# Kernel tuning notes

Hardware: AMD Instinct MI355X
Metric: run time of the kernel (lower is better)

The kernel has to match this reference:

```python
import jax, jax.numpy as jnp
import numpy as np

N = 8192
D = 128
LMBD = 0.1
SPARSITY = 0.99  # fraction of zero entries in A


def setup_inputs() -> dict:
    key = jax.random.key(0)
    kA, kW = jax.random.split(key)
    u = jax.random.uniform(kA, (N, N), dtype=jnp.float32)
    A = jnp.where(u > SPARSITY, u, 0.0)
    W = jax.random.normal(kW, (N, D), dtype=jnp.float32) * 0.02
    b = jnp.zeros((D,), dtype=jnp.float32)
    return {"A": A, "W": W, "b": b}


def reference(A, W, b):
    # model(tf.eye(N)) with Dense(d) == eye(N) @ W + b == W + b  -> [N, d]
    Y = W + b
    # main loss: 0.5 * sum(mask * (A - Y Y^T)^2), mask = (A > 0)
    R = A - jnp.matmul(Y, Y.T)  # [N, N]
    main_loss = 0.5 * jnp.sum(jnp.where(A > 0, R * R, 0.0))
    # reg loss: lmbd/2 * ||Y||_F^2
    reg_loss = 0.5 * LMBD * jnp.sum(Y * Y)
    return main_loss + reg_loss
```

## Files before the change

kernel.cpp:

```cpp
#include <hip/hip_runtime.h>

#define N 8192
#define D 128
#define MAXNZ 256

__device__ __forceinline__ float wave_reduce(float p) {
    #pragma unroll
    for (int off = 32; off > 0; off >>= 1)
        p += __shfl_xor(p, off, 64);
    return p;
}

__global__ __launch_bounds__(256, 8)
void gf_main_kernel(const float* __restrict__ A,
                    const float* __restrict__ W,
                    const float* __restrict__ b,
                    float* __restrict__ partials) {
    __shared__ int   s_col[4][MAXNZ];
    __shared__ float s_val[4][MAXNZ];
    __shared__ float s_bsum[4];

    const int lane = threadIdx.x & 63;
    const int w    = threadIdx.x >> 6;
    const int row  = blockIdx.x * 4 + w;

    const float2 bb = ((const float2*)b)[lane];
    float2 yi = ((const float2*)(W + (size_t)row * D))[lane];
    yi.x += bb.x; yi.y += bb.y;

    const float4* Arow = (const float4*)(A + (size_t)row * N);
    const unsigned long long ltmask = (lane == 63) ? ~0ull >> 1 : (1ull << lane) - 1ull;
    int cnt = 0;
    for (int it = 0; it < N / 256; ++it) {
        const float4 a4 = Arow[it * 64 + lane];
        const float av[4] = {a4.x, a4.y, a4.z, a4.w};
        #pragma unroll
        for (int q = 0; q < 4; ++q) {
            const unsigned long long m = __ballot(av[q] > 0.0f);
            if (av[q] > 0.0f) {
                const int pos = cnt + __popcll(m & ((1ull << lane) - 1ull));
                if (pos < MAXNZ) {
                    s_col[w][pos] = it * 256 + lane * 4 + q;
                    s_val[w][pos] = av[q];
                }
            }
            cnt += __popcll(m);
        }
    }
    if (cnt > MAXNZ) cnt = MAXNZ;
    __syncthreads();

    float acc = 0.0f;
    for (int t = 0; t < cnt; t += 4) {
        float p[4];
        float av[4];
        #pragma unroll
        for (int k = 0; k < 4; ++k) {
            const bool valid = (t + k) < cnt;
            const int  idx   = valid ? (t + k) : 0;
            const int  j     = s_col[w][idx];
            av[k]            = valid ? s_val[w][idx] : 0.0f;
            const float2 yj  = ((const float2*)(W + (size_t)j * D))[lane];
            p[k] = yi.x * (yj.x + bb.x) + yi.y * (yj.y + bb.y);
        }
        #pragma unroll
        for (int off = 32; off > 0; off >>= 1) {
            #pragma unroll
            for (int k = 0; k < 4; ++k)
                p[k] += __shfl_xor(p[k], off, 64);
        }
        #pragma unroll
        for (int k = 0; k < 4; ++k) {
            if ((t + k) < cnt) {
                const float r = av[k] - p[k];
                acc += r * r;
            }
        }
    }

    const float reg = wave_reduce(yi.x * yi.x + yi.y * yi.y);
    const float total = 0.5f * acc + 0.05f * reg;
    if (lane == 0) s_bsum[w] = total;
    __syncthreads();
    if (threadIdx.x == 0)
        partials[blockIdx.x] = s_bsum[0] + s_bsum[1] + s_bsum[2] + s_bsum[3];
}

__global__ __launch_bounds__(256)
void gf_reduce_kernel(const float* __restrict__ partials, float* __restrict__ out) {
    __shared__ float s_ws[4];
    const int lane = threadIdx.x & 63;
    const int w    = threadIdx.x >> 6;
    float s = 0.0f;
    for (int i = threadIdx.x; i < N / 4; i += 256) s += partials[i];
    s = wave_reduce(s);
    if (lane == 0) s_ws[w] = s;
    __syncthreads();
    if (threadIdx.x == 0) out[0] = s_ws[0] + s_ws[1] + s_ws[2] + s_ws[3];
}

extern "C" void kernel_launch(void* const* d_in, const int* in_sizes, int n_in,
                              void* d_out, int out_size, void* d_ws, size_t ws_size,
                              hipStream_t stream) {
    const float* A = (const float*)d_in[0];
    const float* W = (const float*)d_in[1];
    const float* b = (const float*)d_in[2];
    float* out = (float*)d_out;
    float* partials = (float*)d_ws;

    gf_main_kernel<<<dim3(N / 4), dim3(256), 0, stream>>>(A, W, b, partials);
    gf_reduce_kernel<<<dim3(1), dim3(256), 0, stream>>>(partials, out);
}
```

Before: 410.5 us.

## Batch 32 gathered rows and reduce dot products via shared-memory transpose

The per-neighbor dot-product reduction now batches 32 neighbor rows at a time. Each wave writes per-lane partial products into a padded shared-memory tile, then reads it transposed so each half-wave sums a row, finishing with one cross-half shuffle. This replaces four 6-step butterfly shuffle reductions per 4 neighbors, exposes more independent gathers in flight, and defers the final wave reduction to a single pass. It also lowers MAXNZ to 192, drops the occupancy hint from 8 to 4, unrolls the scan loop, and uses about 33KB of LDS, which may reduce occupancy. The MAXNZ cap risks truncating rows with more nonzeros (expected about 82).

```diff
diff --git a/kernel.cpp b/kernel.cpp
--- a/kernel.cpp
+++ b/kernel.cpp
@@ -2,7 +2,9 @@
 
 #define N 8192
 #define D 128
-#define MAXNZ 256
+#define MAXNZ 192
+#define BATCH 32
+#define PPAD 66
 
 __device__ __forceinline__ float wave_reduce(float p) {
     #pragma unroll
@@ -11,13 +13,14 @@
     return p;
 }
 
-__global__ __launch_bounds__(256, 8)
+__global__ __launch_bounds__(256, 4)
 void gf_main_kernel(const float* __restrict__ A,
                     const float* __restrict__ W,
                     const float* __restrict__ b,
                     float* __restrict__ partials) {
     __shared__ int   s_col[4][MAXNZ];
     __shared__ float s_val[4][MAXNZ];
+    __shared__ float s_P[4][BATCH][PPAD];
     __shared__ float s_bsum[4];
 
     const int lane = threadIdx.x & 63;
@@ -29,8 +32,8 @@
     yi.x += bb.x; yi.y += bb.y;
 
     const float4* Arow = (const float4*)(A + (size_t)row * N);
-    const unsigned long long ltmask = (lane == 63) ? ~0ull >> 1 : (1ull << lane) - 1ull;
     int cnt = 0;
+    #pragma unroll 4
     for (int it = 0; it < N / 256; ++it) {
         const float4 a4 = Arow[it * 64 + lane];
         const float av[4] = {a4.x, a4.y, a4.z, a4.w};
@@ -51,35 +54,35 @@
     __syncthreads();
 
     float acc = 0.0f;
-    for (int t = 0; t < cnt; t += 4) {
-        float p[4];
-        float av[4];
+    const int half = lane >> 5;
+    const int sl   = lane & 31;
+
+    for (int base = 0; base < cnt; base += BATCH) {
         #pragma unroll
-        for (int k = 0; k < 4; ++k) {
-            const bool valid = (t + k) < cnt;
-            const int  idx   = valid ? (t + k) : 0;
-            const int  j     = s_col[w][idx];
-            av[k]            = valid ? s_val[w][idx] : 0.0f;
-            const float2 yj  = ((const float2*)(W + (size_t)j * D))[lane];
-            p[k] = yi.x * (yj.x + bb.x) + yi.y * (yj.y + bb.y);
+        for (int k = 0; k < BATCH; ++k) {
+            const int slot = base + k;
+            const int j = (slot < cnt) ? s_col[w][slot] : 0;
+            const float2 yj = ((const float2*)(W + (size_t)j * D))[lane];
+            const float p = yi.x * (yj.x + bb.x) + yi.y * (yj.y + bb.y);
+            s_P[w][k][lane] = p;
         }
+        float ssum = 0.0f;
+        const float2* prow = (const float2*)&s_P[w][sl][half * 32];
         #pragma unroll
-        for (int off = 32; off > 0; off >>= 1) {
-            #pragma unroll
-            for (int k = 0; k < 4; ++k)
-                p[k] += __shfl_xor(p[k], off, 64);
+        for (int t = 0; t < 16; ++t) {
+            const float2 v = prow[t];
+            ssum += v.x + v.y;
         }
-        #pragma unroll
-        for (int k = 0; k < 4; ++k) {
-            if ((t + k) < cnt) {
-                const float r = av[k] - p[k];
-                acc += r * r;
-            }
+        ssum += __shfl_xor(ssum, 32, 64);
+        const int slot = base + sl;
+        if (half == 0 && slot < cnt) {
+            const float r = s_val[w][slot] - ssum;
+            acc += r * r;
         }
     }
 
-    const float reg = wave_reduce(yi.x * yi.x + yi.y * yi.y);
-    const float total = 0.5f * acc + 0.05f * reg;
+    const float v = 0.5f * acc + 0.05f * (yi.x * yi.x + yi.y * yi.y);
+    const float total = wave_reduce(v);
     if (lane == 0) s_bsum[w] = total;
     __syncthreads();
     if (threadIdx.x == 0)
```

Result: no change. 418.1 us (+1.8%).

## Replace sparse gather path with dense bf16 MFMA SDDMM over tiles

Applied to the files above, without the earlier changes.

Replaces per-row nonzero compaction and scattered Y-row gathers with a dense tiled computation of Y·Yᵀ using bf16 MFMA instructions, masking the residual by A>0 as each tile is consumed. A prep kernel converts Y=W+b to bf16 and computes the regularization term separately. This trades extra (cheap) matrix-core FLOPs for regular, coalesced streaming of A and removes the serial ballot/compaction loop, at the cost of reduced precision in the dot products.

```diff
diff --git a/kernel.cpp b/kernel.cpp
--- a/kernel.cpp
+++ b/kernel.cpp
@@ -2,7 +2,15 @@
 
 #define N 8192
 #define D 128
-#define MAXNZ 256
+
+typedef __attribute__((ext_vector_type(8))) short short8;
+typedef __attribute__((ext_vector_type(4))) float float4v;
+
+__device__ __forceinline__ unsigned short f32_to_bf16(float f) {
+    unsigned int u = __float_as_uint(f);
+    unsigned int r = (u + 0x7fffu + ((u >> 16) & 1u)) >> 16;
+    return (unsigned short)r;
+}
 
 __device__ __forceinline__ float wave_reduce(float p) {
     #pragma unroll
@@ -11,88 +19,93 @@
     return p;
 }
 
-__global__ __launch_bounds__(256, 8)
-void gf_main_kernel(const float* __restrict__ A,
-                    const float* __restrict__ W,
-                    const float* __restrict__ b,
-                    float* __restrict__ partials) {
-    __shared__ int   s_col[4][MAXNZ];
-    __shared__ float s_val[4][MAXNZ];
-    __shared__ float s_bsum[4];
+__global__ __launch_bounds__(256)
+void gf_prep_kernel(const float* __restrict__ W, const float* __restrict__ b,
+                    unsigned short* __restrict__ ybf, float* __restrict__ regp) {
+    __shared__ float s_ws[4];
+    const int t = blockIdx.x * 256 + threadIdx.x;
+    const int f = t * 4;
+    const int dcol = f & (D - 1);
+    const float4 wv = *(const float4*)(W + f);
+    const float4 bv = *(const float4*)(b + dcol);
+    const float y0 = wv.x + bv.x, y1 = wv.y + bv.y, y2 = wv.z + bv.z, y3 = wv.w + bv.w;
 
+    ushort4 o;
+    o.x = f32_to_bf16(y0); o.y = f32_to_bf16(y1);
+    o.z = f32_to_bf16(y2); o.w = f32_to_bf16(y3);
+    *(ushort4*)(ybf + f) = o;
+
+    float s = y0*y0 + y1*y1 + y2*y2 + y3*y3;
+    s = wave_reduce(s);
+    const int lane = threadIdx.x & 63, w = threadIdx.x >> 6;
+    if (lane == 0) s_ws[w] = s;
+    __syncthreads();
+    if (threadIdx.x == 0)
+        regp[blockIdx.x] = 0.05f * (s_ws[0] + s_ws[1] + s_ws[2] + s_ws[3]);
+}
+
+__global__ __launch_bounds__(256, 4)
+void gf_sddmm_kernel(const float* __restrict__ A,
+                     const unsigned short* __restrict__ ybf,
+                     float* __restrict__ partials) {
+    __shared__ float s_ws[4];
     const int lane = threadIdx.x & 63;
     const int w    = threadIdx.x >> 6;
-    const int row  = blockIdx.x * 4 + w;
+    const int i0   = blockIdx.x * 128 + w * 32;
+    const int j0   = blockIdx.y * 128;
+    const int r16  = lane & 15;
+    const int quad = lane >> 4;
 
-    const float2 bb = ((const float2*)b)[lane];
-    float2 yi = ((const float2*)(W + (size_t)row * D))[lane];
-    yi.x += bb.x; yi.y += bb.y;
+    short8 afr[2][4];
+    #pragma unroll
+    for (int s = 0; s < 2; ++s) {
+        const unsigned short* yrow = ybf + (size_t)(i0 + s * 16 + r16) * D;
+        #pragma unroll
+        for (int c = 0; c < 4; ++c)
+            afr[s][c] = *(const short8*)(yrow + c * 32 + quad * 8);
+    }
 
-    const float4* Arow = (const float4*)(A + (size_t)row * N);
-    const unsigned long long ltmask = (lane == 63) ? ~0ull >> 1 : (1ull << lane) - 1ull;
-    int cnt = 0;
-    for (int it = 0; it < N / 256; ++it) {
-        const float4 a4 = Arow[it * 64 + lane];
-        const float av[4] = {a4.x, a4.y, a4.z, a4.w};
-        #pragma unroll
-        for (int q = 0; q < 4; ++q) {
-            const unsigned long long m = __ballot(av[q] > 0.0f);
-            if (av[q] > 0.0f) {
-                const int pos = cnt + __popcll(m & ((1ull << lane) - 1ull));
-                if (pos < MAXNZ) {
-                    s_col[w][pos] = it * 256 + lane * 4 + q;
-                    s_val[w][pos] = av[q];
-                }
-            }
-            cnt += __popcll(m);
-        }
-    }
-    if (cnt > MAXNZ) cnt = MAXNZ;
-    __syncthreads();
-
-    float acc = 0.0f;
-    for (int t = 0; t < cnt; t += 4) {
-        float p[4];
-        float av[4];
-        #pragma unroll
-        for (int k = 0; k < 4; ++k) {
-            const bool valid = (t + k) < cnt;
-            const int  idx   = valid ? (t + k) : 0;
-            const int  j     = s_col[w][idx];
-            av[k]            = valid ? s_val[w][idx] : 0.0f;
-            const float2 yj  = ((const float2*)(W + (size_t)j * D))[lane];
-            p[k] = yi.x * (yj.x + bb.x) + yi.y * (yj.y + bb.y);
+    float loss = 0.0f;
+    for (int jj = 0; jj < 8; ++jj) {
+        const int jbase = j0 + jj * 16;
+        short8 bfr[4];
+        {
+            const unsigned short* yrow = ybf + (size_t)(jbase + r16) * D;
+            #pragma unroll
+            for (int c = 0; c < 4; ++c)
+                bfr[c] = *(const short8*)(yrow + c * 32 + quad * 8);
         }
         #pragma unroll
-        for (int off = 32; off > 0; off >>= 1) {
+        for (int s = 0; s < 2; ++s) {
+            float4v acc = {0.f, 0.f, 0.f, 0.f};
             #pragma unroll
-            for (int k = 0; k < 4; ++k)
-                p[k] += __shfl_xor(p[k], off, 64);
-        }
-        #pragma unroll
-        for (int k = 0; k < 4; ++k) {
-            if ((t + k) < cnt) {
-                const float r = av[k] - p[k];
-                acc += r * r;
+            for (int c = 0; c < 4; ++c)
+                acc = __builtin_amdgcn_mfma_f32_16x16x32_bf16(afr[s][c], bfr[c], acc, 0, 0, 0);
+            const int col = jbase + r16;
+            #pragma unroll
+            for (int r = 0; r < 4; ++r) {
+                const int row = i0 + s * 16 + quad * 4 + r;
+                const float a = A[(size_t)row * N + col];
+                const float d = a - acc[r];
+                loss += (a > 0.0f) ? d * d : 0.0f;
             }
         }
     }
 
-    const float reg = wave_reduce(yi.x * yi.x + yi.y * yi.y);
-    const float total = 0.5f * acc + 0.05f * reg;
-    if (lane == 0) s_bsum[w] = total;
+    loss = wave_reduce(loss);
+    if (lane == 0) s_ws[w] = loss;
     __syncthreads();
     if (threadIdx.x == 0)
-        partials[blockIdx.x] = s_bsum[0] + s_bsum[1] + s_bsum[2] + s_bsum[3];
+        partials[blockIdx.y * gridDim.x + blockIdx.x] =
+            0.5f * (s_ws[0] + s_ws[1] + s_ws[2] + s_ws[3]);
 }
 
 __global__ __launch_bounds__(256)
-void gf_reduce_kernel(const float* __restrict__ partials, float* __restrict__ out) {
+void gf_reduce_kernel(const float* __restrict__ parts, float* __restrict__ out) {
     __shared__ float s_ws[4];
-    const int lane = threadIdx.x & 63;
-    const int w    = threadIdx.x >> 6;
+    const int lane = threadIdx.x & 63, w = threadIdx.x >> 6;
     float s = 0.0f;
-    for (int i = threadIdx.x; i < N / 4; i += 256) s += partials[i];
+    for (int i = threadIdx.x; i < 4096 + 1024; i += 256) s += parts[i];
     s = wave_reduce(s);
     if (lane == 0) s_ws[w] = s;
     __syncthreads();
@@ -106,8 +119,11 @@
     const float* W = (const float*)d_in[1];
     const float* b = (const float*)d_in[2];
     float* out = (float*)d_out;
-    float* partials = (float*)d_ws;
 
-    gf_main_kernel<<<dim3(N / 4), dim3(256), 0, stream>>>(A, W, b, partials);
-    gf_reduce_kernel<<<dim3(1), dim3(256), 0, stream>>>(partials, out);
+    float* parts = (float*)d_ws;
+    unsigned short* ybf = (unsigned short*)((float*)d_ws + 8192);
+
+    gf_prep_kernel<<<dim3(N * D / 1024), dim3(256), 0, stream>>>(W, b, ybf, parts + 4096);
+    gf_sddmm_kernel<<<dim3(64, 64), dim3(256), 0, stream>>>(A, ybf, parts);
+    gf_reduce_kernel<<<dim3(1), dim3(256), 0, stream>>>(parts, out);
 }
```

Measured after the change: 435.7 us. 6.1% more time.
